# Kernel optimization log

Hardware: AMD Instinct MI355X
Metric: run time of the kernel (lower is better)

The kernel has to match this reference:

```python
import jax, jax.numpy as jnp
import numpy as np

L = 8        # num_layers
REPEAT = 2   # repeats per layer
DIM = 256    # mixer hidden dim
DIM2 = 128   # head dim (divisible by 32 for AvgPool1d(32))
B = 8192
EPS = 1e-5


def hardswish(x):
    return x * jnp.clip(x + 3.0, 0.0, 6.0) * (1.0 / 6.0)


def layernorm(x, g, b):
    m = jnp.mean(x, axis=-1, keepdims=True)
    xc = x - m
    v = jnp.mean(xc * xc, axis=-1, keepdims=True)
    return xc * jax.lax.rsqrt(v + EPS) * g + b


def setup_inputs() -> dict:
    key = jax.random.key(0)
    ks = jax.random.split(key, 32)
    s = 0.1
    inp = {
        "x": jax.random.normal(ks[0], (B, 3, 32, 32), dtype=jnp.float32),
        "conv_w": jax.random.normal(ks[1], (3,), dtype=jnp.float32) * s,
        "conv_b": jax.random.normal(ks[2], (1,), dtype=jnp.float32) * s,
        "fc0_w": jax.random.normal(ks[3], (32, 32), dtype=jnp.float32) * s,
        "fc0_b": jax.random.normal(ks[4], (32,), dtype=jnp.float32) * s,
        "ln1_g": jnp.ones((L, 32), dtype=jnp.float32),
        "ln1_b": jnp.zeros((L, 32), dtype=jnp.float32),
        "w11": jax.random.normal(ks[5], (L, DIM, 32), dtype=jnp.float32) * s,
        "b11": jax.random.normal(ks[6], (L, DIM), dtype=jnp.float32) * s,
        "w12": jax.random.normal(ks[7], (L, 32, DIM), dtype=jnp.float32) * s,
        "b12": jax.random.normal(ks[8], (L, 32), dtype=jnp.float32) * s,
        "ln2_g": jnp.ones((L, 32), dtype=jnp.float32),
        "ln2_b": jnp.zeros((L, 32), dtype=jnp.float32),
        "w21": jax.random.normal(ks[9], (L, DIM, 32), dtype=jnp.float32) * s,
        "b21": jax.random.normal(ks[10], (L, DIM), dtype=jnp.float32) * s,
        "w22": jax.random.normal(ks[11], (L, 32, DIM), dtype=jnp.float32) * s,
        "b22": jax.random.normal(ks[12], (L, 32), dtype=jnp.float32) * s,
        "fc1_w": jax.random.normal(ks[13], (DIM2, 32), dtype=jnp.float32) * s,
        "fc1_b": jax.random.normal(ks[14], (DIM2,), dtype=jnp.float32) * s,
        "fcout_w": jax.random.normal(ks[15], (10, DIM2), dtype=jnp.float32) * s,
        "fcout_b": jax.random.normal(ks[16], (10,), dtype=jnp.float32) * s,
    }
    return inp


def reference(x, conv_w, conv_b, fc0_w, fc0_b, ln1_g, ln1_b, w11, b11, w12, b12,
              ln2_g, ln2_b, w21, b21, w22, b22, fc1_w, fc1_b, fcout_w, fcout_b):
    # rgb_conv: 1x1 conv 3->1 channels, then squeeze -> [B, 32, 32]
    h = jnp.einsum('bchw,c->bhw', x, conv_w) + conv_b[0]
    h = h @ fc0_w.T + fc0_b  # fc0 over last dim (32)

    for i in range(L):
        for _ in range(REPEAT):
            # token-mixing branch (operates along dim 1 via permute)
            t = layernorm(h, ln1_g[i], ln1_b[i])
            t = jnp.swapaxes(t, 1, 2)                      # [B, 32, 32]
            t = hardswish(t @ w11[i].T + b11[i])           # [B, 32, DIM]
            t = t @ w12[i].T + b12[i]                      # [B, 32, 32]
            h = h + jnp.swapaxes(t, 1, 2)
            # channel-mixing branch
            c = layernorm(h, ln2_g[i], ln2_b[i])
            c = hardswish(c @ w21[i].T + b21[i])           # [B, 32, DIM]
            h = h + (c @ w22[i].T + b22[i])                # [B, 32, 32]

    y = hardswish(h @ fc1_w.T + fc1_b)                     # [B, 32, DIM2]
    # AvgPool1d(kernel=32, stride=32) over last dim -> [B, 32, DIM2//32]
    y = y.reshape(y.shape[0], 32, DIM2 // 32, 32).mean(axis=-1)
    y = y.reshape(y.shape[0], -1)                          # [B, DIM2]
    return y @ fcout_w.T + fcout_b                         # [B, 10]
```

## Files before the change

### kernel.cpp

```cpp
#include <hip/hip_runtime.h>

#define LNUM 8

typedef __attribute__((ext_vector_type(4))) float f32x4;
typedef __attribute__((ext_vector_type(2))) float f32x2;
typedef __attribute__((ext_vector_type(8))) _Float16 f16x8;
typedef __attribute__((ext_vector_type(2))) _Float16 f16x2;

#define MFMAH(A,B,C) __builtin_amdgcn_mfma_f32_16x16x32_f16(A,B,C,0,0,0)
#define PKRTZ(a,b) __builtin_bit_cast(f16x2, __builtin_amdgcn_cvt_pkrtz(a,b))

__device__ __forceinline__ float hswish_clamp(float t) {
  return __builtin_amdgcn_fmed3f(t + 3.f, 0.f, 6.f);
}
__device__ __forceinline__ f16x2 hsw_pk(f16x2 t) {
  const f16x2 c3 = {(_Float16)3.0f, (_Float16)3.0f};
  const f16x2 c0 = {(_Float16)0.0f, (_Float16)0.0f};
  const f16x2 c6 = {(_Float16)6.0f, (_Float16)6.0f};
  f16x2 u = t + c3;
  u = __builtin_elementwise_min(__builtin_elementwise_max(u, c0), c6);
  return t * u;
}

__device__ __forceinline__ int hws(int row, int c) {
  return (row << 5) + ((((c >> 2) ^ (row & 7)) << 2) | (c & 3));
}

__global__ void prep_weights(const float* __restrict__ w11, const float* __restrict__ b11,
                             const float* __restrict__ w12, const float* __restrict__ b12,
                             const float* __restrict__ g1,  const float* __restrict__ be1,
                             const float* __restrict__ w21, const float* __restrict__ b21,
                             const float* __restrict__ w22, const float* __restrict__ b22,
                             const float* __restrict__ g2,  const float* __restrict__ be2,
                             const float* __restrict__ fc1w, const float* __restrict__ fc1b,
                             char* __restrict__ ws)
{
  const int lb = blockIdx.x;
  const int t = threadIdx.x;
  if (lb == 16) {
    char* o = ws + (size_t)16 * 34816;
    _Float16* wf = (_Float16*)o;
    float* pr = (float*)(o + 8192);
    #pragma unroll
    for (int i = 0; i < 2; ++i) {
      int s = t + i*256;
      int lane = s & 63;
      int row = (s >> 6)*16 + (lane & 15);
      int kb  = ((lane >> 4) & 3) * 8;
      const float* src = fc1w + row*32 + kb;
      #pragma unroll
      for (int j = 0; j < 8; ++j) wf[s*8 + j] = (_Float16)src[j];
    }
    if (t < 128) pr[t] = fc1b[t];
    return;
  }
  const int lay = lb >> 1, br = lb & 1;
  const float* w1  = (br ? w21 : w11) + lay*8192;
  const float* w2  = (br ? w22 : w12) + lay*8192;
  const float* bb1 = (br ? b21 : b11) + lay*256;
  const float* bb2 = (br ? b22 : b12) + lay*32;
  const float* gg  = (br ? g2  : g1 ) + lay*32;
  const float* bb  = (br ? be2 : be1) + lay*32;
  char* o = ws + (size_t)lb * 34816;
  _Float16* w1f = (_Float16*)o;
  _Float16* w2f = (_Float16*)(o + 16384);
  float* pr  = (float*)(o + 32768);
  #pragma unroll
  for (int i = 0; i < 4; ++i) {
    int s = t + i*256;
    int lane = s & 63;
    int row = (s >> 6)*16 + (lane & 15);
    int kb  = ((lane >> 4) & 3) * 8;
    const float* src = w1 + row*32 + kb;
    #pragma unroll
    for (int j = 0; j < 8; ++j) w1f[s*8 + j] = (_Float16)src[j];
  }
  #pragma unroll
  for (int i = 0; i < 4; ++i) {
    int s = t + i*256;
    int lane = s & 63;
    int tt = s >> 7;
    int nt = (s >> 6) & 1;
    int n  = nt*16 + (lane & 15);
    int qq = (lane >> 4) & 3;
    const float* src = w2 + n*256 + tt*32 + qq*4;
    _Float16* dst = w2f + s*8;
    #pragma unroll
    for (int j = 0; j < 4; ++j) dst[j]     = (_Float16)(src[j]      * (1.0f/6.0f));
    #pragma unroll
    for (int j = 0; j < 4; ++j) dst[4 + j] = (_Float16)(src[16 + j] * (1.0f/6.0f));
  }
  pr[t] = bb1[t];
  if (t < 32)      pr[256 + t] = bb2[t];
  else if (t < 64) pr[256 + t] = gg[t - 32];
  else if (t < 96) pr[256 + t] = bb[t - 64];
}

__global__ __launch_bounds__(256, 3)
void mixer_mfma(const float* __restrict__ x,
                const float* __restrict__ conv_w, const float* __restrict__ conv_b,
                const float* __restrict__ fc0_w,  const float* __restrict__ fc0_b,
                const char*  __restrict__ ws,
                const float* __restrict__ fcout_w, const float* __restrict__ fcout_b,
                float* __restrict__ out)
{
  __shared__ float smem[4 * 2176];
  const int tid = threadIdx.x;
  const int wv  = tid >> 6;
  const int lid = tid & 63;
  const int ml  = lid & 15;
  const int q   = lid >> 4;
  const int q4  = q << 2, q8 = q << 3;
  const int sl  = lid >> 5, r = lid & 31;
  const int r7  = r & 7;

  float* hW  = smem + wv * 2176;
  float* stW = hW + 2048;

  const size_t b0 = (size_t)blockIdx.x * 8 + (size_t)wv * 2;

  {
    const size_t b = b0 + sl;
    const float* xb = x + b*3072 + r*32;
    const float cw0 = conv_w[0], cw1 = conv_w[1], cw2 = conv_w[2], cb = conv_b[0];
    float g[32];
    #pragma unroll
    for (int j4 = 0; j4 < 8; ++j4) {
      f32x4 a0 = *(const f32x4*)(xb + j4*4);
      f32x4 a1 = *(const f32x4*)(xb + 1024 + j4*4);
      f32x4 a2 = *(const f32x4*)(xb + 2048 + j4*4);
      #pragma unroll
      for (int e = 0; e < 4; ++e)
        g[j4*4+e] = cw0*a0[e] + cw1*a1[e] + cw2*a2[e] + cb;
    }
    f32x4* hp = (f32x4*)(hW + sl*1024 + (r << 5));
    #pragma unroll
    for (int a = 0; a < 8; ++a) {
      f32x4 w;
      #pragma unroll
      for (int e = 0; e < 4; ++e) {
        const int j = a*4 + e;
        const float* wr = fc0_w + j*32;
        float acc = fc0_b[j];
        #pragma unroll
        for (int k = 0; k < 32; ++k) acc += g[k]*wr[k];
        w[e] = acc;
      }
      hp[a ^ r7] = w;
    }
  }

  for (int lay = 0; lay < LNUM; ++lay)
  for (int rep = 0; rep < 2; ++rep)
  for (int br = 0; br < 2; ++br) {
    const char* wsb = ws + (size_t)(lay*2 + br) * 34816;
    const f16x8* w1f = (const f16x8*)wsb;
    const f16x8* w2f = (const f16x8*)(wsb + 16384);
    const float* pb1 = (const float*)(wsb + 32768);
    const float* pb2 = pb1 + 256;
    const float* pg  = pb1 + 288;
    const float* pbt = pb1 + 320;

    {
      const f32x4* hp = (const f32x4*)(hW + sl*1024 + (r << 5));
      float sum = 0.f, sq = 0.f;
      #pragma unroll
      for (int a = 0; a < 8; ++a) {
        f32x4 v = hp[a ^ r7];
        #pragma unroll
        for (int e = 0; e < 4; ++e) { sum += v[e]; sq += v[e]*v[e]; }
      }
      float m = sum * (1.f/32.f);
      float rstd = rsqrtf(sq*(1.f/32.f) - m*m + 1e-5f);
      *(f32x2*)(stW + ((sl << 5) + r)*2) = (f32x2){m, rstd};
    }

    f16x8 b1[4];
    if (br == 0) {
      const float ga = pg[ml],  gb = pg[16 + ml];
      const float ba = pbt[ml], bb2v = pbt[16 + ml];
      #pragma unroll
      for (int i = 0; i < 8; ++i) {
        const int k = q8 + i;
        f32x2 s0 = *(const f32x2*)(stW + k*2);
        f32x2 s1 = *(const f32x2*)(stW + 64 + k*2);
        #pragma unroll
        for (int mt = 0; mt < 4; ++mt) {
          const int samp = mt >> 1;
          const int c = ((mt & 1) << 4) + ml;
          f32x2 st = samp ? s1 : s0;
          float v = hW[samp*1024 + hws(k, c)];
          float g_ = (mt & 1) ? gb : ga;
          float be = (mt & 1) ? bb2v : ba;
          b1[mt][i] = (_Float16)((v - st[0]) * st[1] * g_ + be);
        }
      }
    } else {
      f32x4 g0 = *(const f32x4*)(pg + q8);
      f32x4 g1 = *(const f32x4*)(pg + q8 + 4);
      f32x4 t0 = *(const f32x4*)(pbt + q8);
      f32x4 t1 = *(const f32x4*)(pbt + q8 + 4);
      #pragma unroll
      for (int mt = 0; mt < 4; ++mt) {
        const int samp = mt >> 1;
        const int row = ((mt & 1) << 4) + ml;
        f32x2 st = *(const f32x2*)(stW + ((samp << 5) + row)*2);
        const f32x4* hr = (const f32x4*)(hW + samp*1024 + (row << 5));
        f32x4 v0 = hr[(2*q)     ^ (row & 7)];
        f32x4 v1 = hr[(2*q + 1) ^ (row & 7)];
        #pragma unroll
        for (int e = 0; e < 4; ++e) {
          b1[mt][e]     = (_Float16)((v0[e] - st[0]) * st[1] * g0[e] + t0[e]);
          b1[mt][4 + e] = (_Float16)((v1[e] - st[0]) * st[1] * g1[e] + t1[e]);
        }
      }
    }

    f32x4 acc2[2][4];
    if (br == 0) {
      const float i0 = pb2[ml], i1 = pb2[16 + ml];
      #pragma unroll
      for (int mt = 0; mt < 4; ++mt) {
        acc2[0][mt] = (f32x4){i0, i0, i0, i0};
        acc2[1][mt] = (f32x4){i1, i1, i1, i1};
      }
    } else {
      f32x4 i0 = *(const f32x4*)(pb2 + q4);
      f32x4 i1 = *(const f32x4*)(pb2 + 16 + q4);
      #pragma unroll
      for (int mt = 0; mt < 4; ++mt) { acc2[0][mt] = i0; acc2[1][mt] = i1; }
    }
    #pragma unroll 2
    for (int t = 0; t < 8; ++t) {
      f16x8 a1a = w1f[(t*2 + 0)*64 + lid];
      f16x8 a1b = w1f[(t*2 + 1)*64 + lid];
      f32x4 biasa = *(const f32x4*)(pb1 + t*32 + q4);
      f32x4 biasb = *(const f32x4*)(pb1 + t*32 + 16 + q4);
      f16x8 a2a = w2f[(t*2 + 0)*64 + lid];
      f16x8 a2b = w2f[(t*2 + 1)*64 + lid];
      #pragma unroll
      for (int mt = 0; mt < 4; ++mt) {
        f32x4 c1a = MFMAH(a1a, b1[mt], biasa);
        f32x4 c1b = MFMAH(a1b, b1[mt], biasb);
        union { f16x2 h2[4]; f16x8 v; } b2u;
        b2u.h2[0] = hsw_pk(PKRTZ(c1a[0], c1a[1]));
        b2u.h2[1] = hsw_pk(PKRTZ(c1a[2], c1a[3]));
        b2u.h2[2] = hsw_pk(PKRTZ(c1b[0], c1b[1]));
        b2u.h2[3] = hsw_pk(PKRTZ(c1b[2], c1b[3]));
        if (br == 0) {
          acc2[0][mt] = MFMAH(b2u.v, a2a, acc2[0][mt]);
          acc2[1][mt] = MFMAH(b2u.v, a2b, acc2[1][mt]);
        } else {
          acc2[0][mt] = MFMAH(a2a, b2u.v, acc2[0][mt]);
          acc2[1][mt] = MFMAH(a2b, b2u.v, acc2[1][mt]);
        }
      }
    }

    if (br == 0) {
      #pragma unroll
      for (int mt = 0; mt < 4; ++mt) {
        const int samp = mt >> 1;
        #pragma unroll
        for (int nt = 0; nt < 2; ++nt) {
          const int row = (nt << 4) + ml;
          f32x4* hr = (f32x4*)(hW + samp*1024 + (row << 5));
          const int a = (((mt & 1) << 2) + q) ^ (row & 7);
          f32x4 v = hr[a];
          v += acc2[nt][mt];
          hr[a] = v;
        }
      }
    } else {
      #pragma unroll
      for (int mt = 0; mt < 4; ++mt) {
        const int samp = mt >> 1;
        const int row = ((mt & 1) << 4) + ml;
        f32x4* hr = (f32x4*)(hW + samp*1024 + (row << 5));
        #pragma unroll
        for (int nt = 0; nt < 2; ++nt) {
          const int a = ((nt << 2) + q) ^ (row & 7);
          f32x4 v = hr[a];
          v += acc2[nt][mt];
          hr[a] = v;
        }
      }
    }
  }

  {
    const f16x8* fc1f = (const f16x8*)(ws + (size_t)16 * 34816);
    const float* fb   = (const float*)(ws + (size_t)16 * 34816 + 8192);
    f16x8 be[4];
    #pragma unroll
    for (int mt = 0; mt < 4; ++mt) {
      const int samp = mt >> 1;
      const int row = ((mt & 1) << 4) + ml;
      const f32x4* hr = (const f32x4*)(hW + samp*1024 + (row << 5));
      f32x4 v0 = hr[(2*q)     ^ (row & 7)];
      f32x4 v1 = hr[(2*q + 1) ^ (row & 7)];
      #pragma unroll
      for (int e = 0; e < 4; ++e) {
        be[mt][e]     = (_Float16)v0[e];
        be[mt][4 + e] = (_Float16)v1[e];
      }
    }
    float pl[4][4] = {};
    #pragma unroll
    for (int dt = 0; dt < 8; ++dt) {
      f16x8 af = fc1f[dt*64 + lid];
      f32x4 bias4 = *(const f32x4*)(fb + dt*16 + q4);
      #pragma unroll
      for (int mt = 0; mt < 4; ++mt) {
        f32x4 c = MFMAH(af, be[mt], bias4);
        float s = 0.f;
        #pragma unroll
        for (int rg = 0; rg < 4; ++rg) s += c[rg] * hswish_clamp(c[rg]);
        pl[dt >> 1][mt] += s;
      }
    }
    #pragma unroll
    for (int t = 0; t < 4; ++t)
    #pragma unroll
    for (int mt = 0; mt < 4; ++mt) {
      float v = pl[t][mt];
      v += __shfl_xor(v, 16);
      v += __shfl_xor(v, 32);
      pl[t][mt] = v;
    }
    if (q == 0) {
      #pragma unroll
      for (int mt = 0; mt < 4; ++mt)
      #pragma unroll
      for (int t = 0; t < 4; ++t)
        hW[(mt >> 1)*1024 + (((mt & 1) << 4) + ml)*4 + t] = pl[t][mt];
    }
    if (r < 10) {
      const float* pv = hW + sl*1024;
      const float* wr = fcout_w + r*128;
      float acc = 0.f;
      #pragma unroll
      for (int m4 = 0; m4 < 32; ++m4) {
        f32x4 p4 = *(const f32x4*)(pv + m4*4);
        f32x4 w4 = *(const f32x4*)(wr + m4*4);
        acc += p4[0]*w4[0] + p4[1]*w4[1] + p4[2]*w4[2] + p4[3]*w4[3];
      }
      out[(b0 + sl)*10 + r] = fcout_b[r] + acc * (1.f/192.f);
    }
  }
}

extern "C" void kernel_launch(void* const* d_in, const int* in_sizes, int n_in,
                              void* d_out, int out_size, void* d_ws, size_t ws_size,
                              hipStream_t stream) {
  (void)in_sizes; (void)n_in; (void)out_size; (void)ws_size;
  const float* x       = (const float*)d_in[0];
  const float* conv_w  = (const float*)d_in[1];
  const float* conv_b  = (const float*)d_in[2];
  const float* fc0_w   = (const float*)d_in[3];
  const float* fc0_b   = (const float*)d_in[4];
  const float* ln1_g   = (const float*)d_in[5];
  const float* ln1_b   = (const float*)d_in[6];
  const float* w11     = (const float*)d_in[7];
  const float* b11     = (const float*)d_in[8];
  const float* w12     = (const float*)d_in[9];
  const float* b12     = (const float*)d_in[10];
  const float* ln2_g   = (const float*)d_in[11];
  const float* ln2_b   = (const float*)d_in[12];
  const float* w21     = (const float*)d_in[13];
  const float* b21     = (const float*)d_in[14];
  const float* w22     = (const float*)d_in[15];
  const float* b22     = (const float*)d_in[16];
  const float* fc1_w   = (const float*)d_in[17];
  const float* fc1_b   = (const float*)d_in[18];
  const float* fcout_w = (const float*)d_in[19];
  const float* fcout_b = (const float*)d_in[20];
  float* out = (float*)d_out;
  char* ws = (char*)d_ws;

  prep_weights<<<17, 256, 0, stream>>>(w11, b11, w12, b12, ln1_g, ln1_b,
                                       w21, b21, w22, b22, ln2_g, ln2_b,
                                       fc1_w, fc1_b, ws);
  mixer_mfma<<<1024, 256, 0, stream>>>(x, conv_w, conv_b, fc0_w, fc0_b,
                                       (const char*)ws, fcout_w, fcout_b, out);
}
```

Before: 472.3 us.

## Keep residual stream in registers and transpose via LDS only for token mixing

The residual activations now stay in registers (hreg) for the whole layer loop, laid out to match the MFMA fragment layout. LayerNorm statistics are computed with cross-lane shuffles, and LDS is used only to transpose normalized values for the token-mixing branch. The weight prep is reordered so the K layout matches the register fragments, and hardswish is now computed in fp32 before packing instead of in packed fp16. This removes per-branch LDS round trips of h but adds register pressure and more fp32 ALU work.

```diff
diff --git a/kernel.cpp b/kernel.cpp
--- a/kernel.cpp
+++ b/kernel.cpp
@@ -13,18 +13,7 @@
 __device__ __forceinline__ float hswish_clamp(float t) {
   return __builtin_amdgcn_fmed3f(t + 3.f, 0.f, 6.f);
 }
-__device__ __forceinline__ f16x2 hsw_pk(f16x2 t) {
-  const f16x2 c3 = {(_Float16)3.0f, (_Float16)3.0f};
-  const f16x2 c0 = {(_Float16)0.0f, (_Float16)0.0f};
-  const f16x2 c6 = {(_Float16)6.0f, (_Float16)6.0f};
-  f16x2 u = t + c3;
-  u = __builtin_elementwise_min(__builtin_elementwise_max(u, c0), c6);
-  return t * u;
-}
-
-__device__ __forceinline__ int hws(int row, int c) {
-  return (row << 5) + ((((c >> 2) ^ (row & 7)) << 2) | (c & 3));
-}
+
 
 __global__ void prep_weights(const float* __restrict__ w11, const float* __restrict__ b11,
                              const float* __restrict__ w12, const float* __restrict__ b12,
@@ -46,10 +35,12 @@
       int s = t + i*256;
       int lane = s & 63;
       int row = (s >> 6)*16 + (lane & 15);
-      int kb  = ((lane >> 4) & 3) * 8;
-      const float* src = fc1w + row*32 + kb;
-      #pragma unroll
-      for (int j = 0; j < 8; ++j) wf[s*8 + j] = (_Float16)src[j];
+      int qq  = (lane >> 4) & 3;
+      const float* src = fc1w + row*32;
+      #pragma unroll
+      for (int j = 0; j < 4; ++j) wf[s*8 + j]     = (_Float16)src[4*qq + j];
+      #pragma unroll
+      for (int j = 0; j < 4; ++j) wf[s*8 + 4 + j] = (_Float16)src[16 + 4*qq + j];
     }
     if (t < 128) pr[t] = fc1b[t];
     return;
@@ -70,10 +61,12 @@
     int s = t + i*256;
     int lane = s & 63;
     int row = (s >> 6)*16 + (lane & 15);
-    int kb  = ((lane >> 4) & 3) * 8;
-    const float* src = w1 + row*32 + kb;
-    #pragma unroll
-    for (int j = 0; j < 8; ++j) w1f[s*8 + j] = (_Float16)src[j];
+    int qq  = (lane >> 4) & 3;
+    const float* src = w1 + row*32;
+    #pragma unroll
+    for (int j = 0; j < 4; ++j) w1f[s*8 + j]     = (_Float16)src[4*qq + j];
+    #pragma unroll
+    for (int j = 0; j < 4; ++j) w1f[s*8 + 4 + j] = (_Float16)src[16 + 4*qq + j];
   }
   #pragma unroll
   for (int i = 0; i < 4; ++i) {
@@ -104,20 +97,20 @@
                 const float* __restrict__ fcout_w, const float* __restrict__ fcout_b,
                 float* __restrict__ out)
 {
-  __shared__ float smem[4 * 2176];
+  __shared__ float smem[4 * 2048];
   const int tid = threadIdx.x;
   const int wv  = tid >> 6;
   const int lid = tid & 63;
   const int ml  = lid & 15;
   const int q   = lid >> 4;
-  const int q4  = q << 2, q8 = q << 3;
+  const int q4  = q << 2;
   const int sl  = lid >> 5, r = lid & 31;
-  const int r7  = r & 7;
-
-  float* hW  = smem + wv * 2176;
-  float* stW = hW + 2048;
+
+  float* W = smem + wv * 2048;
 
   const size_t b0 = (size_t)blockIdx.x * 8 + (size_t)wv * 2;
+
+  f32x4 hreg[2][2][2];
 
   {
     const size_t b = b0 + sl;
@@ -133,7 +126,8 @@
       for (int e = 0; e < 4; ++e)
         g[j4*4+e] = cw0*a0[e] + cw1*a1[e] + cw2*a2[e] + cb;
     }
-    f32x4* hp = (f32x4*)(hW + sl*1024 + (r << 5));
+    float* hs = W + sl*1024;
+    const int rsw = 2*((r >> 2) & 3) + (r & 3);
     #pragma unroll
     for (int a = 0; a < 8; ++a) {
       f32x4 w;
@@ -146,144 +140,209 @@
         for (int k = 0; k < 32; ++k) acc += g[k]*wr[k];
         w[e] = acc;
       }
-      hp[a ^ r7] = w;
+      *(f32x4*)(hs + r*32 + ((a + rsw) & 7)*4) = w;
+    }
+  }
+  {
+    const int c2r = 2*(ml >> 2) + (ml & 3);
+    #pragma unroll
+    for (int s = 0; s < 2; ++s)
+    #pragma unroll
+    for (int a = 0; a < 2; ++a) {
+      const int row = a*16 + ml;
+      #pragma unroll
+      for (int b_ = 0; b_ < 2; ++b_)
+        hreg[s][a][b_] = *(const f32x4*)(W + s*1024 + row*32 + (((b_*4 + q) + c2r) & 7)*4);
     }
   }
 
   for (int lay = 0; lay < LNUM; ++lay)
-  for (int rep = 0; rep < 2; ++rep)
-  for (int br = 0; br < 2; ++br) {
-    const char* wsb = ws + (size_t)(lay*2 + br) * 34816;
-    const f16x8* w1f = (const f16x8*)wsb;
-    const f16x8* w2f = (const f16x8*)(wsb + 16384);
-    const float* pb1 = (const float*)(wsb + 32768);
-    const float* pb2 = pb1 + 256;
-    const float* pg  = pb1 + 288;
-    const float* pbt = pb1 + 320;
+  for (int rep = 0; rep < 2; ++rep) {
 
     {
-      const f32x4* hp = (const f32x4*)(hW + sl*1024 + (r << 5));
-      float sum = 0.f, sq = 0.f;
-      #pragma unroll
-      for (int a = 0; a < 8; ++a) {
-        f32x4 v = hp[a ^ r7];
-        #pragma unroll
-        for (int e = 0; e < 4; ++e) { sum += v[e]; sq += v[e]*v[e]; }
-      }
-      float m = sum * (1.f/32.f);
-      float rstd = rsqrtf(sq*(1.f/32.f) - m*m + 1e-5f);
-      *(f32x2*)(stW + ((sl << 5) + r)*2) = (f32x2){m, rstd};
-    }
-
-    f16x8 b1[4];
-    if (br == 0) {
-      const float ga = pg[ml],  gb = pg[16 + ml];
-      const float ba = pbt[ml], bb2v = pbt[16 + ml];
-      #pragma unroll
-      for (int i = 0; i < 8; ++i) {
-        const int k = q8 + i;
-        f32x2 s0 = *(const f32x2*)(stW + k*2);
-        f32x2 s1 = *(const f32x2*)(stW + 64 + k*2);
+      const char* wsb = ws + (size_t)(lay*2) * 34816;
+      const f16x8* w1f = (const f16x8*)wsb;
+      const f16x8* w2f = (const f16x8*)(wsb + 16384);
+      const float* pb1 = (const float*)(wsb + 32768);
+      const float* pb2 = pb1 + 256;
+      const float* pg  = pb1 + 288;
+      const float* pbt = pb1 + 320;
+
+      float mean_[2][2], rstd_[2][2];
+      #pragma unroll
+      for (int s = 0; s < 2; ++s)
+      #pragma unroll
+      for (int a = 0; a < 2; ++a) {
+        f32x4 v0 = hreg[s][a][0], v1 = hreg[s][a][1];
+        float sum = (v0[0]+v0[1])+(v0[2]+v0[3])+(v1[0]+v1[1])+(v1[2]+v1[3]);
+        float sq  = v0[0]*v0[0]+v0[1]*v0[1]+v0[2]*v0[2]+v0[3]*v0[3]
+                  + v1[0]*v1[0]+v1[1]*v1[1]+v1[2]*v1[2]+v1[3]*v1[3];
+        sum += __shfl_xor(sum, 16); sum += __shfl_xor(sum, 32);
+        sq  += __shfl_xor(sq, 16);  sq  += __shfl_xor(sq, 32);
+        float m = sum * (1.f/32.f);
+        mean_[s][a] = m;
+        rstd_[s][a] = rsqrtf(sq*(1.f/32.f) - m*m + 1e-5f);
+      }
+      #pragma unroll
+      for (int s = 0; s < 2; ++s) {
+        float* hs = W + s*1024;
+        #pragma unroll
+        for (int a = 0; a < 2; ++a) {
+          const float m_ = mean_[s][a], rs = rstd_[s][a];
+          #pragma unroll
+          for (int b_ = 0; b_ < 2; ++b_)
+          #pragma unroll
+          for (int e = 0; e < 4; ++e) {
+            const int rowR = b_*16 + q4 + e;
+            const int cw = ((a*4 + (ml >> 2)) + 2*q + e) & 7;
+            hs[rowR*32 + cw*4 + (ml & 3)] = (hreg[s][a][b_][e] - m_) * rs;
+          }
+        }
+      }
+      f16x8 b1[4];
+      #pragma unroll
+      for (int mt = 0; mt < 4; ++mt) {
+        const int s = mt >> 1, ch = mt & 1;
+        const float* hs = W + s*1024;
+        const int crow = ch*16 + ml;
+        const int c2 = 2*(ml >> 2) + (ml & 3);
+        f32x4 v0 = *(const f32x4*)(hs + crow*32 + ((q + c2) & 7)*4);
+        f32x4 v1 = *(const f32x4*)(hs + crow*32 + ((4 + q + c2) & 7)*4);
+        const float gc = pg[crow], bc = pbt[crow];
+        #pragma unroll
+        for (int e = 0; e < 4; ++e) {
+          b1[mt][e]     = (_Float16)(v0[e] * gc + bc);
+          b1[mt][4 + e] = (_Float16)(v1[e] * gc + bc);
+        }
+      }
+      f32x4 acc2[2][4];
+      {
+        const float i0 = pb2[ml], i1 = pb2[16 + ml];
         #pragma unroll
         for (int mt = 0; mt < 4; ++mt) {
-          const int samp = mt >> 1;
-          const int c = ((mt & 1) << 4) + ml;
-          f32x2 st = samp ? s1 : s0;
-          float v = hW[samp*1024 + hws(k, c)];
-          float g_ = (mt & 1) ? gb : ga;
-          float be = (mt & 1) ? bb2v : ba;
-          b1[mt][i] = (_Float16)((v - st[0]) * st[1] * g_ + be);
-        }
-      }
-    } else {
-      f32x4 g0 = *(const f32x4*)(pg + q8);
-      f32x4 g1 = *(const f32x4*)(pg + q8 + 4);
-      f32x4 t0 = *(const f32x4*)(pbt + q8);
-      f32x4 t1 = *(const f32x4*)(pbt + q8 + 4);
-      #pragma unroll
-      for (int mt = 0; mt < 4; ++mt) {
-        const int samp = mt >> 1;
-        const int row = ((mt & 1) << 4) + ml;
-        f32x2 st = *(const f32x2*)(stW + ((samp << 5) + row)*2);
-        const f32x4* hr = (const f32x4*)(hW + samp*1024 + (row << 5));
-        f32x4 v0 = hr[(2*q)     ^ (row & 7)];
-        f32x4 v1 = hr[(2*q + 1) ^ (row & 7)];
-        #pragma unroll
-        for (int e = 0; e < 4; ++e) {
-          b1[mt][e]     = (_Float16)((v0[e] - st[0]) * st[1] * g0[e] + t0[e]);
-          b1[mt][4 + e] = (_Float16)((v1[e] - st[0]) * st[1] * g1[e] + t1[e]);
-        }
-      }
-    }
-
-    f32x4 acc2[2][4];
-    if (br == 0) {
-      const float i0 = pb2[ml], i1 = pb2[16 + ml];
-      #pragma unroll
-      for (int mt = 0; mt < 4; ++mt) {
-        acc2[0][mt] = (f32x4){i0, i0, i0, i0};
-        acc2[1][mt] = (f32x4){i1, i1, i1, i1};
-      }
-    } else {
-      f32x4 i0 = *(const f32x4*)(pb2 + q4);
-      f32x4 i1 = *(const f32x4*)(pb2 + 16 + q4);
-      #pragma unroll
-      for (int mt = 0; mt < 4; ++mt) { acc2[0][mt] = i0; acc2[1][mt] = i1; }
-    }
-    #pragma unroll 2
-    for (int t = 0; t < 8; ++t) {
-      f16x8 a1a = w1f[(t*2 + 0)*64 + lid];
-      f16x8 a1b = w1f[(t*2 + 1)*64 + lid];
-      f32x4 biasa = *(const f32x4*)(pb1 + t*32 + q4);
-      f32x4 biasb = *(const f32x4*)(pb1 + t*32 + 16 + q4);
-      f16x8 a2a = w2f[(t*2 + 0)*64 + lid];
-      f16x8 a2b = w2f[(t*2 + 1)*64 + lid];
-      #pragma unroll
-      for (int mt = 0; mt < 4; ++mt) {
-        f32x4 c1a = MFMAH(a1a, b1[mt], biasa);
-        f32x4 c1b = MFMAH(a1b, b1[mt], biasb);
-        union { f16x2 h2[4]; f16x8 v; } b2u;
-        b2u.h2[0] = hsw_pk(PKRTZ(c1a[0], c1a[1]));
-        b2u.h2[1] = hsw_pk(PKRTZ(c1a[2], c1a[3]));
-        b2u.h2[2] = hsw_pk(PKRTZ(c1b[0], c1b[1]));
-        b2u.h2[3] = hsw_pk(PKRTZ(c1b[2], c1b[3]));
-        if (br == 0) {
+          acc2[0][mt] = (f32x4){i0, i0, i0, i0};
+          acc2[1][mt] = (f32x4){i1, i1, i1, i1};
+        }
+      }
+      #pragma unroll 2
+      for (int t = 0; t < 8; ++t) {
+        f16x8 a1a = w1f[(t*2 + 0)*64 + lid];
+        f16x8 a1b = w1f[(t*2 + 1)*64 + lid];
+        f32x4 biasa = *(const f32x4*)(pb1 + t*32 + q4);
+        f32x4 biasb = *(const f32x4*)(pb1 + t*32 + 16 + q4);
+        f16x8 a2a = w2f[(t*2 + 0)*64 + lid];
+        f16x8 a2b = w2f[(t*2 + 1)*64 + lid];
+        #pragma unroll
+        for (int mt = 0; mt < 4; ++mt) {
+          f32x4 c1a = MFMAH(a1a, b1[mt], biasa);
+          f32x4 c1b = MFMAH(a1b, b1[mt], biasb);
+          float va0 = c1a[0]*hswish_clamp(c1a[0]);
+          float va1 = c1a[1]*hswish_clamp(c1a[1]);
+          float va2 = c1a[2]*hswish_clamp(c1a[2]);
+          float va3 = c1a[3]*hswish_clamp(c1a[3]);
+          float vb0 = c1b[0]*hswish_clamp(c1b[0]);
+          float vb1 = c1b[1]*hswish_clamp(c1b[1]);
+          float vb2 = c1b[2]*hswish_clamp(c1b[2]);
+          float vb3 = c1b[3]*hswish_clamp(c1b[3]);
+          union { f16x2 h2[4]; f16x8 v; } b2u;
+          b2u.h2[0] = PKRTZ(va0, va1);
+          b2u.h2[1] = PKRTZ(va2, va3);
+          b2u.h2[2] = PKRTZ(vb0, vb1);
+          b2u.h2[3] = PKRTZ(vb2, vb3);
           acc2[0][mt] = MFMAH(b2u.v, a2a, acc2[0][mt]);
           acc2[1][mt] = MFMAH(b2u.v, a2b, acc2[1][mt]);
-        } else {
+        }
+      }
+      #pragma unroll
+      for (int mt = 0; mt < 4; ++mt) {
+        const int s = mt >> 1, mtc = mt & 1;
+        #pragma unroll
+        for (int nt = 0; nt < 2; ++nt)
+          hreg[s][nt][mtc] += acc2[nt][mt];
+      }
+    }
+
+    {
+      const char* wsb = ws + (size_t)(lay*2 + 1) * 34816;
+      const f16x8* w1f = (const f16x8*)wsb;
+      const f16x8* w2f = (const f16x8*)(wsb + 16384);
+      const float* pb1 = (const float*)(wsb + 32768);
+      const float* pb2 = pb1 + 256;
+      const float* pg  = pb1 + 288;
+      const float* pbt = pb1 + 320;
+
+      float mean_[2][2], rstd_[2][2];
+      #pragma unroll
+      for (int s = 0; s < 2; ++s)
+      #pragma unroll
+      for (int a = 0; a < 2; ++a) {
+        f32x4 v0 = hreg[s][a][0], v1 = hreg[s][a][1];
+        float sum = (v0[0]+v0[1])+(v0[2]+v0[3])+(v1[0]+v1[1])+(v1[2]+v1[3]);
+        float sq  = v0[0]*v0[0]+v0[1]*v0[1]+v0[2]*v0[2]+v0[3]*v0[3]
+                  + v1[0]*v1[0]+v1[1]*v1[1]+v1[2]*v1[2]+v1[3]*v1[3];
+        sum += __shfl_xor(sum, 16); sum += __shfl_xor(sum, 32);
+        sq  += __shfl_xor(sq, 16);  sq  += __shfl_xor(sq, 32);
+        float m = sum * (1.f/32.f);
+        mean_[s][a] = m;
+        rstd_[s][a] = rsqrtf(sq*(1.f/32.f) - m*m + 1e-5f);
+      }
+      f16x8 b1[4];
+      f32x4 g0v = *(const f32x4*)(pg + q4);
+      f32x4 g1v = *(const f32x4*)(pg + 16 + q4);
+      f32x4 t0v = *(const f32x4*)(pbt + q4);
+      f32x4 t1v = *(const f32x4*)(pbt + 16 + q4);
+      #pragma unroll
+      for (int mt = 0; mt < 4; ++mt) {
+        const int s = mt >> 1, a = mt & 1;
+        const float m_ = mean_[s][a], rs = rstd_[s][a];
+        #pragma unroll
+        for (int e = 0; e < 4; ++e) {
+          b1[mt][e]     = (_Float16)((hreg[s][a][0][e] - m_) * rs * g0v[e] + t0v[e]);
+          b1[mt][4 + e] = (_Float16)((hreg[s][a][1][e] - m_) * rs * g1v[e] + t1v[e]);
+        }
+      }
+      f32x4 acc2[2][4];
+      {
+        f32x4 i0 = *(const f32x4*)(pb2 + q4);
+        f32x4 i1 = *(const f32x4*)(pb2 + 16 + q4);
+        #pragma unroll
+        for (int mt = 0; mt < 4; ++mt) { acc2[0][mt] = i0; acc2[1][mt] = i1; }
+      }
+      #pragma unroll 2
+      for (int t = 0; t < 8; ++t) {
+        f16x8 a1a = w1f[(t*2 + 0)*64 + lid];
+        f16x8 a1b = w1f[(t*2 + 1)*64 + lid];
+        f32x4 biasa = *(const f32x4*)(pb1 + t*32 + q4);
+        f32x4 biasb = *(const f32x4*)(pb1 + t*32 + 16 + q4);
+        f16x8 a2a = w2f[(t*2 + 0)*64 + lid];
+        f16x8 a2b = w2f[(t*2 + 1)*64 + lid];
+        #pragma unroll
+        for (int mt = 0; mt < 4; ++mt) {
+          f32x4 c1a = MFMAH(a1a, b1[mt], biasa);
+          f32x4 c1b = MFMAH(a1b, b1[mt], biasb);
+          float va0 = c1a[0]*hswish_clamp(c1a[0]);
+          float va1 = c1a[1]*hswish_clamp(c1a[1]);
+          float va2 = c1a[2]*hswish_clamp(c1a[2]);
+          float va3 = c1a[3]*hswish_clamp(c1a[3]);
+          float vb0 = c1b[0]*hswish_clamp(c1b[0]);
+          float vb1 = c1b[1]*hswish_clamp(c1b[1]);
+          float vb2 = c1b[2]*hswish_clamp(c1b[2]);
+          float vb3 = c1b[3]*hswish_clamp(c1b[3]);
+          union { f16x2 h2[4]; f16x8 v; } b2u;
+          b2u.h2[0] = PKRTZ(va0, va1);
+          b2u.h2[1] = PKRTZ(va2, va3);
+          b2u.h2[2] = PKRTZ(vb0, vb1);
+          b2u.h2[3] = PKRTZ(vb2, vb3);
           acc2[0][mt] = MFMAH(a2a, b2u.v, acc2[0][mt]);
           acc2[1][mt] = MFMAH(a2b, b2u.v, acc2[1][mt]);
         }
       }
-    }
-
-    if (br == 0) {
       #pragma unroll
       for (int mt = 0; mt < 4; ++mt) {
-        const int samp = mt >> 1;
-        #pragma unroll
-        for (int nt = 0; nt < 2; ++nt) {
-          const int row = (nt << 4) + ml;
-          f32x4* hr = (f32x4*)(hW + samp*1024 + (row << 5));
-          const int a = (((mt & 1) << 2) + q) ^ (row & 7);
-          f32x4 v = hr[a];
-          v += acc2[nt][mt];
-          hr[a] = v;
-        }
-      }
-    } else {
-      #pragma unroll
-      for (int mt = 0; mt < 4; ++mt) {
-        const int samp = mt >> 1;
-        const int row = ((mt & 1) << 4) + ml;
-        f32x4* hr = (f32x4*)(hW + samp*1024 + (row << 5));
-        #pragma unroll
-        for (int nt = 0; nt < 2; ++nt) {
-          const int a = ((nt << 2) + q) ^ (row & 7);
-          f32x4 v = hr[a];
-          v += acc2[nt][mt];
-          hr[a] = v;
-        }
+        const int s = mt >> 1, a = mt & 1;
+        #pragma unroll
+        for (int nt = 0; nt < 2; ++nt)
+          hreg[s][a][nt] += acc2[nt][mt];
       }
     }
   }
@@ -294,15 +353,11 @@
     f16x8 be[4];
     #pragma unroll
     for (int mt = 0; mt < 4; ++mt) {
-      const int samp = mt >> 1;
-      const int row = ((mt & 1) << 4) + ml;
-      const f32x4* hr = (const f32x4*)(hW + samp*1024 + (row << 5));
-      f32x4 v0 = hr[(2*q)     ^ (row & 7)];
-      f32x4 v1 = hr[(2*q + 1) ^ (row & 7)];
+      const int s = mt >> 1, a = mt & 1;
       #pragma unroll
       for (int e = 0; e < 4; ++e) {
-        be[mt][e]     = (_Float16)v0[e];
-        be[mt][4 + e] = (_Float16)v1[e];
+        be[mt][e]     = (_Float16)hreg[s][a][0][e];
+        be[mt][4 + e] = (_Float16)hreg[s][a][1][e];
       }
     }
     float pl[4][4] = {};
@@ -333,10 +388,10 @@
       for (int mt = 0; mt < 4; ++mt)
       #pragma unroll
       for (int t = 0; t < 4; ++t)
-        hW[(mt >> 1)*1024 + (((mt & 1) << 4) + ml)*4 + t] = pl[t][mt];
+        W[(mt >> 1)*1024 + (((mt & 1) << 4) + ml)*4 + t] = pl[t][mt];
     }
     if (r < 10) {
-      const float* pv = hW + sl*1024;
+      const float* pv = W + sl*1024;
       const float* wr = fcout_w + r*128;
       float acc = 0.f;
       #pragma unroll
```

After: 455.0 us. 3.7% less time.
